# Kernel optimization log

Measured on AMD Instinct MI355X. Metric: run time of the kernel, lower is better.

## Reference

```python
import jax, jax.numpy as jnp
import numpy as np

B, S, HID, H, DK = 16, 1024, 512, 8, 64
NEG = -1e30


def setup_inputs() -> dict:
    key = jax.random.key(0)
    kx, kl, kq, kk, kv, ko = jax.random.split(key, 6)
    x = jax.random.normal(kx, (B, S, HID), dtype=jnp.float32)
    # mask is a prefix of ones per sample (the torch code fills nmask[i, :nsum, :nsum])
    lengths = jax.random.randint(kl, (B,), S // 2, S + 1)
    mask = (jnp.arange(S)[None, :] < lengths[:, None]).astype(jnp.int32)
    scale = 0.02
    Wq = jax.random.normal(kq, (H, HID, DK), dtype=jnp.float32) * scale  # stacked per-head Linear weights
    Wk = jax.random.normal(kk, (H, HID, DK), dtype=jnp.float32) * scale
    Wv = jax.random.normal(kv, (H, HID, DK), dtype=jnp.float32) * scale
    Wout = jax.random.normal(ko, (H * DK, HID), dtype=jnp.float32) * scale
    return {"x": x, "mask": mask, "Wq": Wq, "Wk": Wk, "Wv": Wv, "Wout": Wout}


def reference(x, mask, Wq, Wk, Wv, Wout):
    # x: [B,S,HID], mask: [B,S] int prefix mask
    nsum = mask.sum(-1).astype(jnp.float32)          # [B]
    valid = mask.astype(bool)                         # [B,S]
    pair = valid[:, :, None] & valid[:, None, :]      # [B,S,S] == nmask from the torch loop
    # batched per-head projections (equivalent to the per-head Linear loop)
    Q = jnp.einsum('bsh,nhd->bnsd', x, Wq)            # [B,H,S,DK]
    K = jnp.einsum('bsh,nhd->bnsd', x, Wk)
    V = jnp.einsum('bsh,nhd->bnsd', x, Wv)
    scores = jnp.einsum('bnqd,bnkd->bnqk', Q, K)      # [B,H,S,S]
    scores = scores / jnp.sqrt(nsum)[:, None, None, None]  # per-sample sqrt(len) scale
    scores = jnp.where(pair[:, None, :, :], scores, NEG)   # masked_softmax: -1e30 at masked slots
    p = jax.nn.softmax(scores, axis=-1)
    attn = jnp.einsum('bnqk,bnkd->bnqd', p, V)        # [B,H,S,DK]
    h = attn.transpose(0, 2, 1, 3).reshape(B, S, H * DK)  # concat heads along feature dim
    return jnp.einsum('bsf,fh->bsh', h, Wout)         # W_out, no bias
```

## Files before the change

### kernel.cpp

```cpp
#include <hip/hip_runtime.h>
#include <math.h>

constexpr int CB = 16;
constexpr int CS = 1024;
constexpr int CHID = 512;
constexpr int CH = 8;
constexpr int CDK = 64;

typedef _Float16 f16;
typedef __attribute__((ext_vector_type(8))) _Float16 f16x8;
typedef __attribute__((ext_vector_type(4))) _Float16 f16x4;
typedef __attribute__((ext_vector_type(4))) float f32x4;

__device__ inline f32x4 mfma16(f16x8 a, f16x8 b, f32x4 c) {
  return __builtin_amdgcn_mfma_f32_16x16x32_f16(a, b, c, 0, 0, 0);
}

__device__ inline void gld16(const void* g, void* l) {
  __builtin_amdgcn_global_load_lds(
      (const __attribute__((address_space(1))) void*)g,
      (__attribute__((address_space(3))) void*)l, 16, 0, 0);
}

__device__ inline float fast_exp2(float x) {
#if __has_builtin(__builtin_amdgcn_exp2f)
  return __builtin_amdgcn_exp2f(x);
#else
  return __expf(x * 0.6931471805599453f);
#endif
}

#define LOG2E 1.4426950408889634f

__global__ __launch_bounds__(256) void prep_kernel(const float4* __restrict__ x,
                                                   f16x4* __restrict__ xh,
                                                   const int* __restrict__ mask,
                                                   int* __restrict__ lens,
                                                   float* __restrict__ Vsum) {
  const int bid = blockIdx.x, t = threadIdx.x;
  __shared__ int red[256];
  if (bid < 8192) {
    const int idx = bid * 256 + t;
    const float4 v = x[idx];
    f16x4 o;
    o[0] = (f16)v.x; o[1] = (f16)v.y; o[2] = (f16)v.z; o[3] = (f16)v.w;
    xh[idx] = o;
  } else {
    const int b = bid - 8192;
    const int g = b * 256 + t;
    Vsum[g * 2] = 0.f;
    Vsum[g * 2 + 1] = 0.f;
    int s = 0;
    for (int i = t; i < CS; i += 256) s += mask[b * CS + i];
    red[t] = s;
    __syncthreads();
    for (int off = 128; off > 0; off >>= 1) {
      if (t < off) red[t] += red[t + off];
      __syncthreads();
    }
    if (t == 0) lens[b] = red[0];
  }
}

__global__ __launch_bounds__(256) void cast_w_kernel(const float* __restrict__ Wq,
                                                     const float* __restrict__ Wk,
                                                     const float* __restrict__ Wv,
                                                     const float* __restrict__ Wout,
                                                     f16* __restrict__ wtAll) {
  const int y = blockIdx.y, kb = blockIdx.x, t = threadIdx.x;
  const int k0 = kb * 64;
  const float* src;
  int ldsrc;
  f16* dst;
  if (y < 24) {
    const int which = y >> 3, h = y & 7;
    const float* W = (which == 0) ? Wq : (which == 1) ? Wk : Wv;
    src = W + (size_t)h * 32768 + (size_t)k0 * 64;
    ldsrc = 64;
    dst = wtAll + (size_t)which * 262144 + (size_t)h * 32768;
  } else {
    const int c = y - 24;
    src = Wout + (size_t)k0 * 512 + c * 64;
    ldsrc = 512;
    dst = wtAll + (size_t)3 * 262144 + (size_t)c * 64 * 512;
  }

  __shared__ float Ts[64][68];
  {
    const int kr = t >> 4, cg = (t & 15) * 4;
#pragma unroll
    for (int rr = 0; rr < 4; ++rr) {
      const float4 v = *(const float4*)&src[(size_t)(rr * 16 + kr) * ldsrc + cg];
      Ts[rr * 16 + kr][cg] = v.x;
      Ts[rr * 16 + kr][cg + 1] = v.y;
      Ts[rr * 16 + kr][cg + 2] = v.z;
      Ts[rr * 16 + kr][cg + 3] = v.w;
    }
  }
  __syncthreads();
  {
    const int n = t >> 2, seg = t & 3;
    f16x8 a, b;
#pragma unroll
    for (int j = 0; j < 8; ++j) {
      a[j] = (f16)Ts[seg * 16 + j][n];
      b[j] = (f16)Ts[seg * 16 + 8 + j][n];
    }
    f16* d = &dst[(size_t)n * 512 + k0 + seg * 16];
    *(f16x8*)d = a;
    *(f16x8*)(d + 8) = b;
  }
}

__global__ __launch_bounds__(256) void qkvf_kernel(
    const f16* __restrict__ xh, const f16* __restrict__ wtAll,
    const int* __restrict__ lens, f16* __restrict__ Qh, f16* __restrict__ Kh,
    f16* __restrict__ Vth, float* __restrict__ Vsum) {
  const int ct = blockIdx.x, rt = blockIdx.y;
  const int which = ct >> 2, hp = ct & 3;
  const f16* Wt = wtAll + (size_t)which * 262144 + (size_t)hp * 65536;
  const int row0 = rt * 128;
  const int b = row0 >> 10, s0 = row0 & 1023;
  const int h0 = hp * 2;
  const int t = threadIdx.x;
  const int w = t >> 6, lane = t & 63, quad = lane >> 4, lcol = lane & 15;
  const int wr = w >> 1, wc = w & 1;

  __shared__ union SM {
    struct { f16 Xs[128][64]; f16 Ws[128][64]; } a;
    f16 Ts[128][136];
  } sm;

  f32x4 acc[4][4];
#pragma unroll
  for (int i = 0; i < 4; ++i)
#pragma unroll
    for (int j = 0; j < 4; ++j) acc[i][j] = (f32x4){0.f, 0.f, 0.f, 0.f};

  for (int k0 = 0; k0 < CHID; k0 += 64) {
    __syncthreads();
#pragma unroll
    for (int i = 0; i < 4; ++i) {
      const int c = t + 256 * i, r = c >> 3, sg = c & 7;
      const int gsw = (sg ^ (r & 7)) * 8;
      gld16(&xh[(size_t)(row0 + r) * CHID + k0 + gsw],
            (char*)&sm.a.Xs[0][0] + c * 16);
      gld16(&Wt[(size_t)r * CHID + k0 + gsw], (char*)&sm.a.Ws[0][0] + c * 16);
    }
    __syncthreads();

    f16x8 bf0[4], bf1[4];
#pragma unroll
    for (int j = 0; j < 4; ++j) {
      const int br = wc * 64 + j * 16 + lcol;
      bf0[j] = *(const f16x8*)&sm.a.Ws[br][(quad ^ (br & 7)) * 8];
      bf1[j] = *(const f16x8*)&sm.a.Ws[br][((quad ^ 4) ^ (br & 7)) * 8];
    }
#pragma unroll
    for (int i = 0; i < 4; ++i) {
      const int ar = wr * 64 + i * 16 + lcol;
      const f16x8 af0 = *(const f16x8*)&sm.a.Xs[ar][(quad ^ (ar & 7)) * 8];
      const f16x8 af1 =
          *(const f16x8*)&sm.a.Xs[ar][((quad ^ 4) ^ (ar & 7)) * 8];
#pragma unroll
      for (int j = 0; j < 4; ++j) {
        acc[i][j] = mfma16(af0, bf0[j], acc[i][j]);
        acc[i][j] = mfma16(af1, bf1[j], acc[i][j]);
      }
    }
  }

  if (which == 2) {
#pragma unroll
    for (int j = 0; j < 4; ++j) {
      float ps = 0.f;
#pragma unroll
      for (int i = 0; i < 4; ++i)
#pragma unroll
        for (int rr = 0; rr < 4; ++rr) ps += acc[i][j][rr];
      ps += __shfl_xor(ps, 16);
      ps += __shfl_xor(ps, 32);
      if (quad == 0) {
        const int d128 = wc * 64 + j * 16 + lcol;
        const int h = h0 + (d128 >> 6), d = d128 & 63;
        atomicAdd(&Vsum[((size_t)b * CH + h) * CDK + d], ps);
      }
    }
    __syncthreads();
#pragma unroll
    for (int i = 0; i < 4; ++i)
#pragma unroll
      for (int j = 0; j < 4; ++j) {
        f16x4 v4;
#pragma unroll
        for (int rr = 0; rr < 4; ++rr) v4[rr] = (f16)acc[i][j][rr];
        *(f16x4*)&sm.Ts[wc * 64 + j * 16 + lcol][wr * 64 + i * 16 + quad * 4] =
            v4;
      }
    __syncthreads();
    const int c16 = t & 15;
#pragma unroll
    for (int p = 0; p < 8; ++p) {
      const int vr = p * 16 + (t >> 4);
      const int h = h0 + (vr >> 6), d = vr & 63;
      *(f16x8*)&Vth[(((size_t)b * CH + h) * CDK + d) * CS + s0 + c16 * 8] =
          *(const f16x8*)&sm.Ts[vr][c16 * 8];
    }
  } else {
    const float qsc = (which == 0) ? rsqrtf((float)lens[b]) * LOG2E : 1.0f;
    __syncthreads();
#pragma unroll
    for (int i = 0; i < 4; ++i)
#pragma unroll
      for (int j = 0; j < 4; ++j)
#pragma unroll
        for (int rr = 0; rr < 4; ++rr)
          sm.Ts[wr * 64 + i * 16 + quad * 4 + rr][wc * 64 + j * 16 + lcol] =
              (f16)(acc[i][j][rr] * qsc);
    __syncthreads();
    f16* O = (which == 0) ? Qh : Kh;
    const int c8 = t & 7;
#pragma unroll
    for (int p = 0; p < 4; ++p) {
      const int row = p * 32 + (t >> 3);
#pragma unroll
      for (int half = 0; half < 2; ++half) {
        const int h = h0 + half;
        *(f16x8*)&O[(((size_t)b * CH + h) * CS + s0 + row) * CDK + c8 * 8] =
            *(const f16x8*)&sm.Ts[row][half * 64 + c8 * 8];
      }
    }
  }
}

__global__ __launch_bounds__(256) void attn_kernel(
    const f16* __restrict__ Qh, const f16* __restrict__ Kh,
    const f16* __restrict__ Vth, const int* __restrict__ lens,
    const float* __restrict__ Vsum, f16* __restrict__ Hbh) {
  const int qt = blockIdx.x, h = blockIdx.y, b = blockIdx.z;
  const int n = lens[b];
  const int t = threadIdx.x, w = t >> 6, lane = t & 63, quad = lane >> 4,
            lcol = lane & 15;

  const size_t bh = ((size_t)b * CH + h) * CS;
  const size_t bhd = ((size_t)b * CH + h) * CDK;

  const int nt = (n + 63) >> 6;

  __shared__ f16 Ks[64][72];
  __shared__ f16 Vs[64][72];
  __shared__ f16 Pt[4][32][72];

  const int qbase = qt * 128 + w * 32;
  f16x8 qa[2][2];
#pragma unroll
  for (int set = 0; set < 2; ++set) {
    const size_t qr = bh + qbase + set * 16 + lcol;
    qa[set][0] = *(const f16x8*)&Qh[qr * CDK + quad * 8];
    qa[set][1] = *(const f16x8*)&Qh[qr * CDK + 32 + quad * 8];
  }

  f32x4 o[2][4];
#pragma unroll
  for (int set = 0; set < 2; ++set)
#pragma unroll
    for (int dt = 0; dt < 4; ++dt) o[set][dt] = (f32x4){0.f, 0.f, 0.f, 0.f};
  float lp[2][4] = {{0.f, 0.f, 0.f, 0.f}, {0.f, 0.f, 0.f, 0.f}};

  f16x8 pk[2], pv[2];
#pragma unroll
  for (int i = 0; i < 2; ++i) {
    const int c = t + 256 * i, r = c >> 3, sg = c & 7;
    pk[i] = *(const f16x8*)&Kh[(bh + r) * CDK + sg * 8];
    pv[i] = *(const f16x8*)&Vth[(bhd + r) * CS + sg * 8];
  }

  for (int kt = 0; kt < nt; ++kt) {
    __syncthreads();
#pragma unroll
    for (int i = 0; i < 2; ++i) {
      const int c = t + 256 * i, r = c >> 3, sg = c & 7;
      *(f16x8*)&Ks[r][sg * 8] = pk[i];
      *(f16x8*)&Vs[r][sg * 8] = pv[i];
    }
    __syncthreads();
    const int ktn = (kt + 1 < nt) ? kt + 1 : kt;
#pragma unroll
    for (int i = 0; i < 2; ++i) {
      const int c = t + 256 * i, r = c >> 3, sg = c & 7;
      pk[i] = *(const f16x8*)&Kh[(bh + ktn * 64 + r) * CDK + sg * 8];
      pv[i] = *(const f16x8*)&Vth[(bhd + r) * CS + ktn * 64 + sg * 8];
    }

#pragma unroll
    for (int set = 0; set < 2; ++set) {
      f32x4 st[4];
#pragma unroll
      for (int ct = 0; ct < 4; ++ct) {
        const f16x8 kb0 = *(const f16x8*)&Ks[ct * 16 + lcol][quad * 8];
        const f16x8 kb1 = *(const f16x8*)&Ks[ct * 16 + lcol][32 + quad * 8];
        st[ct] = mfma16(qa[set][0], kb0, (f32x4){0.f, 0.f, 0.f, 0.f});
        st[ct] = mfma16(qa[set][1], kb1, st[ct]);
      }
#pragma unroll
      for (int ct = 0; ct < 4; ++ct) {
        const bool kvld = (kt * 64 + ct * 16 + lcol) < n;
#pragma unroll
        for (int r = 0; r < 4; ++r) {
          float p = fast_exp2(st[ct][r]);
          p = kvld ? p : 0.f;
          lp[set][r] += p;
          Pt[w][set * 16 + quad * 4 + r][ct * 16 + lcol] = (f16)p;
        }
      }
    }

    f16x8 pa[2][2];
#pragma unroll
    for (int set = 0; set < 2; ++set) {
      pa[set][0] = *(const f16x8*)&Pt[w][set * 16 + lcol][quad * 8];
      pa[set][1] = *(const f16x8*)&Pt[w][set * 16 + lcol][32 + quad * 8];
    }

#pragma unroll
    for (int dt = 0; dt < 4; ++dt) {
      const f16x8 vb0 = *(const f16x8*)&Vs[dt * 16 + lcol][quad * 8];
      const f16x8 vb1 = *(const f16x8*)&Vs[dt * 16 + lcol][32 + quad * 8];
#pragma unroll
      for (int set = 0; set < 2; ++set) {
        o[set][dt] = mfma16(pa[set][0], vb0, o[set][dt]);
        o[set][dt] = mfma16(pa[set][1], vb1, o[set][dt]);
      }
    }
  }

  float invl[2][4];
#pragma unroll
  for (int set = 0; set < 2; ++set)
#pragma unroll
    for (int r = 0; r < 4; ++r) {
      float v = lp[set][r];
      v += __shfl_xor(v, 1);
      v += __shfl_xor(v, 2);
      v += __shfl_xor(v, 4);
      v += __shfl_xor(v, 8);
      invl[set][r] = 1.0f / v;
    }

#pragma unroll
  for (int set = 0; set < 2; ++set)
#pragma unroll
    for (int dt = 0; dt < 4; ++dt)
#pragma unroll
      for (int r = 0; r < 4; ++r) {
        const int srow_l = set * 16 + quad * 4 + r;
        const int d = dt * 16 + lcol;
        const float val = (qbase + srow_l < n)
                              ? o[set][dt][r] * invl[set][r]
                              : Vsum[bhd + d] * (1.0f / 1024.0f);
        Pt[w][srow_l][d] = (f16)val;
      }
  {
    const int lr = lane >> 3, lc = lane & 7;
#pragma unroll
    for (int p = 0; p < 4; ++p) {
      const int row = p * 8 + lr;
      *(f16x8*)&Hbh[((size_t)b * CS + qbase + row) * (CH * CDK) + h * CDK +
                    lc * 8] = *(const f16x8*)&Pt[w][row][lc * 8];
    }
  }
}

__global__ __launch_bounds__(256) void outp_kernel(const f16* __restrict__ Hbh,
                                                   const f16* __restrict__ woutt,
                                                   float* __restrict__ out) {
  const int rt = blockIdx.x, ctile = blockIdx.y;
  const int row0 = rt * 128, col0 = ctile * 128;
  const f16* Wt = woutt + (size_t)col0 * CHID;
  const int t = threadIdx.x;
  const int w = t >> 6, lane = t & 63, quad = lane >> 4, lcol = lane & 15;
  const int wr = w >> 1, wc = w & 1;

  __shared__ f16 Hs[128][64];
  __shared__ f16 Ws[128][64];

  f32x4 acc[4][4];
#pragma unroll
  for (int i = 0; i < 4; ++i)
#pragma unroll
    for (int j = 0; j < 4; ++j) acc[i][j] = (f32x4){0.f, 0.f, 0.f, 0.f};

  for (int k0 = 0; k0 < CHID; k0 += 64) {
    __syncthreads();
#pragma unroll
    for (int i = 0; i < 4; ++i) {
      const int c = t + 256 * i, r = c >> 3, sg = c & 7;
      const int gsw = (sg ^ (r & 7)) * 8;
      gld16(&Hbh[(size_t)(row0 + r) * CHID + k0 + gsw],
            (char*)&Hs[0][0] + c * 16);
      gld16(&Wt[(size_t)r * CHID + k0 + gsw], (char*)&Ws[0][0] + c * 16);
    }
    __syncthreads();

    f16x8 bf0[4], bf1[4];
#pragma unroll
    for (int j = 0; j < 4; ++j) {
      const int br = wc * 64 + j * 16 + lcol;
      bf0[j] = *(const f16x8*)&Ws[br][(quad ^ (br & 7)) * 8];
      bf1[j] = *(const f16x8*)&Ws[br][((quad ^ 4) ^ (br & 7)) * 8];
    }
#pragma unroll
    for (int i = 0; i < 4; ++i) {
      const int ar = wr * 64 + i * 16 + lcol;
      const f16x8 af0 = *(const f16x8*)&Hs[ar][(quad ^ (ar & 7)) * 8];
      const f16x8 af1 = *(const f16x8*)&Hs[ar][((quad ^ 4) ^ (ar & 7)) * 8];
#pragma unroll
      for (int j = 0; j < 4; ++j) {
        acc[i][j] = mfma16(af0, bf0[j], acc[i][j]);
        acc[i][j] = mfma16(af1, bf1[j], acc[i][j]);
      }
    }
  }

#pragma unroll
  for (int i = 0; i < 4; ++i) {
#pragma unroll
    for (int rr = 0; rr < 4; ++rr) {
      const size_t rg = row0 + wr * 64 + i * 16 + quad * 4 + rr;
#pragma unroll
      for (int j = 0; j < 4; ++j)
        out[rg * CHID + col0 + wc * 64 + j * 16 + lcol] = acc[i][j][rr];
    }
  }
}

extern "C" void kernel_launch(void* const* d_in, const int* in_sizes, int n_in,
                              void* d_out, int out_size, void* d_ws,
                              size_t ws_size, hipStream_t stream) {
  const float* x = (const float*)d_in[0];
  const int* mask = (const int*)d_in[1];
  const float* Wq = (const float*)d_in[2];
  const float* Wk = (const float*)d_in[3];
  const float* Wv = (const float*)d_in[4];
  const float* Wout = (const float*)d_in[5];
  float* out = (float*)d_out;

  char* ws = (char*)d_ws;
  int* lens = (int*)ws;
  size_t off = 1024;
  const size_t NX = (size_t)CB * CS * CHID;
  const size_t NW = (size_t)CH * CHID * CDK;
  f16* xh = (f16*)(ws + off);    off += NX * 2;
  f16* wtAll = (f16*)(ws + off); off += NW * 4 * 2;
  f16* Qh = (f16*)(ws + off);    off += NX * 2;
  f16* Kh = (f16*)(ws + off);    off += NX * 2;
  f16* Vth = (f16*)(ws + off);   off += NX * 2;
  f16* Hbh = (f16*)(ws + off);   off += NX * 2;
  float* Vsum = (float*)(ws + off); off += (size_t)CB * CH * CDK * 4;
  f16* woutt = wtAll + NW * 3;

  prep_kernel<<<8208, 256, 0, stream>>>((const float4*)x, (f16x4*)xh, mask,
                                        lens, Vsum);
  cast_w_kernel<<<dim3(8, 32), 256, 0, stream>>>(Wq, Wk, Wv, Wout, wtAll);
  qkvf_kernel<<<dim3(12, 128), 256, 0, stream>>>(xh, wtAll, lens, Qh, Kh, Vth,
                                                 Vsum);
  attn_kernel<<<dim3(CS / 128, CH, CB), 256, 0, stream>>>(Qh, Kh, Vth, lens,
                                                          Vsum, Hbh);
  outp_kernel<<<dim3(128, 4), 256, 0, stream>>>(Hbh, woutt, out);
}
```

Measured before the change: 202.3 us.

## Keep attention probabilities in registers via permlane transpose and double-buffer K/V

The QK^T MFMA operands are swapped so each lane holds the scores for one query across keys. The exponentiated probabilities are packed to fp16 and rearranged with permlane32/16 swaps into the A operand for the PV MFMA, so the per-iteration round trip through shared memory for P is gone. K/V tiles are double-buffered in shared memory, with one barrier per iteration instead of two, and the output staging buffer is aliased onto the K/V buffers through a union. Row-sum reduction moves to cross-quad shuffles, and launch bounds now request 4 blocks per CU, which may cap register use and cause spills.

```diff
diff --git a/kernel.cpp b/kernel.cpp
--- a/kernel.cpp
+++ b/kernel.cpp
@@ -11,6 +11,8 @@
 typedef __attribute__((ext_vector_type(8))) _Float16 f16x8;
 typedef __attribute__((ext_vector_type(4))) _Float16 f16x4;
 typedef __attribute__((ext_vector_type(4))) float f32x4;
+typedef __attribute__((ext_vector_type(4))) unsigned int u32x4;
+typedef __attribute__((ext_vector_type(2))) unsigned int u32x2;
 
 __device__ inline f32x4 mfma16(f16x8 a, f16x8 b, f32x4 c) {
   return __builtin_amdgcn_mfma_f32_16x16x32_f16(a, b, c, 0, 0, 0);
@@ -27,6 +29,31 @@
   return __builtin_amdgcn_exp2f(x);
 #else
   return __expf(x * 0.6931471805599453f);
+#endif
+}
+
+__device__ inline unsigned pack_rne(float a, float b) {
+  union { f16 h[2]; unsigned u; } c;
+  c.h[0] = (f16)a;
+  c.h[1] = (f16)b;
+  return c.u;
+}
+
+__device__ inline void quad_transpose(unsigned& x, unsigned& y) {
+#if __has_builtin(__builtin_amdgcn_permlane32_swap) && \
+    __has_builtin(__builtin_amdgcn_permlane16_swap)
+  u32x2 a = __builtin_amdgcn_permlane32_swap(x, y, false, false);
+  u32x2 b = __builtin_amdgcn_permlane16_swap(a[0], a[1], false, false);
+  x = b[0];
+  y = b[1];
+#else
+  asm volatile(
+      "s_nop 1\n\t"
+      "v_permlane32_swap_b32 %0, %1\n\t"
+      "s_nop 1\n\t"
+      "v_permlane16_swap_b32 %0, %1\n\t"
+      "s_nop 1"
+      : "+v"(x), "+v"(y));
 #endif
 }
 
@@ -233,7 +260,7 @@
   }
 }
 
-__global__ __launch_bounds__(256) void attn_kernel(
+__global__ __launch_bounds__(256, 4) void attn_kernel(
     const f16* __restrict__ Qh, const f16* __restrict__ Kh,
     const f16* __restrict__ Vth, const int* __restrict__ lens,
     const float* __restrict__ Vsum, f16* __restrict__ Hbh) {
@@ -247,9 +274,10 @@
 
   const int nt = (n + 63) >> 6;
 
-  __shared__ f16 Ks[64][72];
-  __shared__ f16 Vs[64][72];
-  __shared__ f16 Pt[4][32][72];
+  __shared__ union SM {
+    struct { f16 Ks[2][64][72]; f16 Vs[2][64][72]; } kv;
+    f16 St[4][32][72];
+  } sm;
 
   const int qbase = qt * 128 + w * 32;
   f16x8 qa[2][2];
@@ -265,7 +293,7 @@
   for (int set = 0; set < 2; ++set)
 #pragma unroll
     for (int dt = 0; dt < 4; ++dt) o[set][dt] = (f32x4){0.f, 0.f, 0.f, 0.f};
-  float lp[2][4] = {{0.f, 0.f, 0.f, 0.f}, {0.f, 0.f, 0.f, 0.f}};
+  float lp[2] = {0.f, 0.f};
 
   f16x8 pk[2], pv[2];
 #pragma unroll
@@ -274,16 +302,16 @@
     pk[i] = *(const f16x8*)&Kh[(bh + r) * CDK + sg * 8];
     pv[i] = *(const f16x8*)&Vth[(bhd + r) * CS + sg * 8];
   }
+#pragma unroll
+  for (int i = 0; i < 2; ++i) {
+    const int c = t + 256 * i, r = c >> 3, sg = c & 7;
+    *(f16x8*)&sm.kv.Ks[0][r][sg * 8] = pk[i];
+    *(f16x8*)&sm.kv.Vs[0][r][sg * 8] = pv[i];
+  }
+  __syncthreads();
 
   for (int kt = 0; kt < nt; ++kt) {
-    __syncthreads();
-#pragma unroll
-    for (int i = 0; i < 2; ++i) {
-      const int c = t + 256 * i, r = c >> 3, sg = c & 7;
-      *(f16x8*)&Ks[r][sg * 8] = pk[i];
-      *(f16x8*)&Vs[r][sg * 8] = pv[i];
-    }
-    __syncthreads();
+    const int cur = kt & 1, nxt = cur ^ 1;
     const int ktn = (kt + 1 < nt) ? kt + 1 : kt;
 #pragma unroll
     for (int i = 0; i < 2; ++i) {
@@ -292,60 +320,78 @@
       pv[i] = *(const f16x8*)&Vth[(bhd + r) * CS + ktn * 64 + sg * 8];
     }
 
+    f16x8 pa[2][2];
 #pragma unroll
     for (int set = 0; set < 2; ++set) {
       f32x4 st[4];
 #pragma unroll
       for (int ct = 0; ct < 4; ++ct) {
-        const f16x8 kb0 = *(const f16x8*)&Ks[ct * 16 + lcol][quad * 8];
-        const f16x8 kb1 = *(const f16x8*)&Ks[ct * 16 + lcol][32 + quad * 8];
-        st[ct] = mfma16(qa[set][0], kb0, (f32x4){0.f, 0.f, 0.f, 0.f});
-        st[ct] = mfma16(qa[set][1], kb1, st[ct]);
-      }
-#pragma unroll
-      for (int ct = 0; ct < 4; ++ct) {
-        const bool kvld = (kt * 64 + ct * 16 + lcol) < n;
+        const f16x8 kb0 = *(const f16x8*)&sm.kv.Ks[cur][ct * 16 + lcol][quad * 8];
+        const f16x8 kb1 =
+            *(const f16x8*)&sm.kv.Ks[cur][ct * 16 + lcol][32 + quad * 8];
+        st[ct] = mfma16(kb0, qa[set][0], (f32x4){0.f, 0.f, 0.f, 0.f});
+        st[ct] = mfma16(kb1, qa[set][1], st[ct]);
+      }
+      unsigned pkd[4][2];
+      float ls = 0.f;
+#pragma unroll
+      for (int c = 0; c < 4; ++c) {
+        float p[4];
 #pragma unroll
         for (int r = 0; r < 4; ++r) {
-          float p = fast_exp2(st[ct][r]);
-          p = kvld ? p : 0.f;
-          lp[set][r] += p;
-          Pt[w][set * 16 + quad * 4 + r][ct * 16 + lcol] = (f16)p;
+          const bool kvld = (kt * 64 + c * 16 + quad * 4 + r) < n;
+          float e = fast_exp2(st[c][r]);
+          e = kvld ? e : 0.f;
+          ls += e;
+          p[r] = e;
         }
-      }
-    }
-
-    f16x8 pa[2][2];
-#pragma unroll
-    for (int set = 0; set < 2; ++set) {
-      pa[set][0] = *(const f16x8*)&Pt[w][set * 16 + lcol][quad * 8];
-      pa[set][1] = *(const f16x8*)&Pt[w][set * 16 + lcol][32 + quad * 8];
+        pkd[c][0] = pack_rne(p[0], p[1]);
+        pkd[c][1] = pack_rne(p[2], p[3]);
+      }
+      lp[set] += ls;
+#pragma unroll
+      for (int half = 0; half < 2; ++half) {
+        unsigned x0 = pkd[2 * half][0], y0 = pkd[2 * half + 1][0];
+        unsigned x1 = pkd[2 * half][1], y1 = pkd[2 * half + 1][1];
+        quad_transpose(x0, y0);
+        quad_transpose(x1, y1);
+        union { u32x4 u; f16x8 h; } cc;
+        cc.u = (u32x4){x0, x1, y0, y1};
+        pa[set][half] = cc.h;
+      }
     }
 
 #pragma unroll
     for (int dt = 0; dt < 4; ++dt) {
-      const f16x8 vb0 = *(const f16x8*)&Vs[dt * 16 + lcol][quad * 8];
-      const f16x8 vb1 = *(const f16x8*)&Vs[dt * 16 + lcol][32 + quad * 8];
+      const f16x8 vb0 = *(const f16x8*)&sm.kv.Vs[cur][dt * 16 + lcol][quad * 8];
+      const f16x8 vb1 =
+          *(const f16x8*)&sm.kv.Vs[cur][dt * 16 + lcol][32 + quad * 8];
 #pragma unroll
       for (int set = 0; set < 2; ++set) {
         o[set][dt] = mfma16(pa[set][0], vb0, o[set][dt]);
         o[set][dt] = mfma16(pa[set][1], vb1, o[set][dt]);
       }
     }
+
+#pragma unroll
+    for (int i = 0; i < 2; ++i) {
+      const int c = t + 256 * i, r = c >> 3, sg = c & 7;
+      *(f16x8*)&sm.kv.Ks[nxt][r][sg * 8] = pk[i];
+      *(f16x8*)&sm.kv.Vs[nxt][r][sg * 8] = pv[i];
+    }
+    __syncthreads();
   }
 
   float invl[2][4];
 #pragma unroll
-  for (int set = 0; set < 2; ++set)
-#pragma unroll
-    for (int r = 0; r < 4; ++r) {
-      float v = lp[set][r];
-      v += __shfl_xor(v, 1);
-      v += __shfl_xor(v, 2);
-      v += __shfl_xor(v, 4);
-      v += __shfl_xor(v, 8);
-      invl[set][r] = 1.0f / v;
-    }
+  for (int set = 0; set < 2; ++set) {
+    float v = lp[set];
+    v += __shfl_xor(v, 16);
+    v += __shfl_xor(v, 32);
+#pragma unroll
+    for (int r = 0; r < 4; ++r)
+      invl[set][r] = 1.0f / __shfl(v, (lane & 48) | (quad * 4 + r));
+  }
 
 #pragma unroll
   for (int set = 0; set < 2; ++set)
@@ -358,7 +404,7 @@
         const float val = (qbase + srow_l < n)
                               ? o[set][dt][r] * invl[set][r]
                               : Vsum[bhd + d] * (1.0f / 1024.0f);
-        Pt[w][srow_l][d] = (f16)val;
+        sm.St[w][srow_l][d] = (f16)val;
       }
   {
     const int lr = lane >> 3, lc = lane & 7;
@@ -366,7 +412,7 @@
     for (int p = 0; p < 4; ++p) {
       const int row = p * 8 + lr;
       *(f16x8*)&Hbh[((size_t)b * CS + qbase + row) * (CH * CDK) + h * CDK +
-                    lc * 8] = *(const f16x8*)&Pt[w][row][lc * 8];
+                    lc * 8] = *(const f16x8*)&sm.St[w][row][lc * 8];
     }
   }
 }
```

After: 196.6 us. -2.8%, faster.
